# Performance work log

Measured on AMD Instinct MI355X. Metric: run time of the kernel, lower is better.

Reference implementation:

```python
import jax, jax.numpy as jnp
import numpy as np

H = 32  # d_model
EPS = 1e-5  # LayerNorm eps (PyTorch default)


def _lstm_layer(x, W_ih, W_hh, b_ih, b_hh):
    """Single LSTM layer, batch_first x: (B, T, D) -> ys: (B, T, H).
    PyTorch gate order: i, f, g, o."""
    B, T, _ = x.shape
    # Hoist the input projection out of the recurrence: one big GEMM.
    xg = jnp.einsum('btd,gd->btg', x, W_ih) + b_ih + b_hh  # (B, T, 4H)
    xg = jnp.swapaxes(xg, 0, 1)  # (T, B, 4H) for scan over time

    def step(carry, xg_t):
        h, c = carry
        gates = xg_t + h @ W_hh.T  # (B, 4H)
        i, f, g, o = jnp.split(gates, 4, axis=-1)
        i = jax.nn.sigmoid(i)
        f = jax.nn.sigmoid(f)
        g = jnp.tanh(g)
        o = jax.nn.sigmoid(o)
        c = f * c + i * g
        h = o * jnp.tanh(c)
        return (h, c), h

    h0 = jnp.zeros((B, H), dtype=x.dtype)
    c0 = jnp.zeros((B, H), dtype=x.dtype)
    (_, _), ys = jax.lax.scan(step, (h0, c0), xg)
    return jnp.swapaxes(ys, 0, 1)  # (B, T, H)


def setup_inputs() -> dict:
    key = jax.random.key(0)
    ks = jax.random.split(key, 10)
    B, T, D = 4096, 512, 6
    s = 1.0 / np.sqrt(H)  # PyTorch LSTM init scale
    inp = {
        'x': jax.random.normal(ks[0], (B, T, D), dtype=jnp.float32),
        # layer 0: input_dim=6 -> H
        'W_ih0': jax.random.uniform(ks[1], (4 * H, D), minval=-s, maxval=s, dtype=jnp.float32),
        'W_hh0': jax.random.uniform(ks[2], (4 * H, H), minval=-s, maxval=s, dtype=jnp.float32),
        'b_ih0': jax.random.uniform(ks[3], (4 * H,), minval=-s, maxval=s, dtype=jnp.float32),
        'b_hh0': jax.random.uniform(ks[4], (4 * H,), minval=-s, maxval=s, dtype=jnp.float32),
        # layer 1: H -> H
        'W_ih1': jax.random.uniform(ks[5], (4 * H, H), minval=-s, maxval=s, dtype=jnp.float32),
        'W_hh1': jax.random.uniform(ks[6], (4 * H, H), minval=-s, maxval=s, dtype=jnp.float32),
        'b_ih1': jax.random.uniform(ks[7], (4 * H,), minval=-s, maxval=s, dtype=jnp.float32),
        'b_hh1': jax.random.uniform(ks[8], (4 * H,), minval=-s, maxval=s, dtype=jnp.float32),
        # final LayerNorm params
        'ln_gamma': jnp.ones((H,), dtype=jnp.float32),
        'ln_beta': jnp.zeros((H,), dtype=jnp.float32),
    }
    return inp


def reference(x, W_ih0, W_hh0, b_ih0, b_hh0, W_ih1, W_hh1, b_ih1, b_hh1, ln_gamma, ln_beta):
    # Two-layer LSTM (dropout between layers is a no-op in eval mode).
    h1 = _lstm_layer(x, W_ih0, W_hh0, b_ih0, b_hh0)   # (B, T, H)
    h2 = _lstm_layer(h1, W_ih1, W_hh1, b_ih1, b_hh1)  # (B, T, H)
    last = h2[:, -1, :]  # (B, H)
    mu = jnp.mean(last, axis=-1, keepdims=True)
    var = jnp.var(last, axis=-1, keepdims=True)
    return (last - mu) / jnp.sqrt(var + EPS) * ln_gamma + ln_beta
```

## Files before the change

kernel.cpp:

```cpp
#include <hip/hip_runtime.h>

#define TT   512
#define DD   6
#define HD   32
#define CH   32
#define EPSL 1e-5f

typedef _Float16 half8 __attribute__((ext_vector_type(8)));
typedef __attribute__((ext_vector_type(4))) float f32x4;

#define MFMA_F16(a, b, c) __builtin_amdgcn_mfma_f32_16x16x32_f16((a), (b), (c), 0, 0, 0)

__global__ __launch_bounds__(256, 1) void lstm2_pipe(
    const float* __restrict__ x,
    const float* __restrict__ W_ih0,
    const float* __restrict__ W_hh0,
    const float* __restrict__ b_ih0,
    const float* __restrict__ b_hh0,
    const float* __restrict__ W_ih1,
    const float* __restrict__ W_hh1,
    const float* __restrict__ b_ih1,
    const float* __restrict__ b_hh1,
    const float* __restrict__ gamma,
    const float* __restrict__ beta,
    float* __restrict__ out)
{
    const int tid = threadIdx.x;
    const int w   = tid >> 6;
    const int L   = w >> 1;
    const int uh  = w & 1;
    const int ln  = tid & 63;
    const int q   = ln >> 4;
    const int n   = ln & 15;
    const int u   = 16 * uh + n;
    const int b0  = blockIdx.x << 4;

    __shared__ __align__(16) _Float16 h0r[2][16][40];
    __shared__ __align__(16) _Float16 h1r[2][16][40];
    __shared__ __align__(16) _Float16 xs[2][CH][16][8];
    __shared__ float ln_s[16][33];

    {
        unsigned* p0 = (unsigned*)&h0r[0][0][0];
        for (int i = tid; i < (int)(sizeof(h0r) / 4); i += 256) p0[i] = 0u;
        unsigned* p1 = (unsigned*)&h1r[0][0][0];
        for (int i = tid; i < (int)(sizeof(h1r) / 4); i += 256) p1[i] = 0u;
        unsigned* p2 = (unsigned*)&xs[0][0][0][0];
        for (int i = tid; i < (int)(sizeof(xs) / 4); i += 256) p2[i] = 0u;
    }

    const float* Wa = L ? W_ih1 : W_hh0;
    const float* bi = L ? b_ih1 : b_ih0;
    const float* bh = L ? b_hh1 : b_hh0;

#define SETUP(p, SC) \
    half8 Ba##p, Bb##p; float K##p; { \
        const int g = 32 * (p) + u; \
        const float4* r4 = (const float4*)(Wa + g * 32 + 8 * q); \
        float4 va = r4[0], vb = r4[1]; \
        Ba##p = half8{(_Float16)(SC * va.x), (_Float16)(SC * va.y), \
                      (_Float16)(SC * va.z), (_Float16)(SC * va.w), \
                      (_Float16)(SC * vb.x), (_Float16)(SC * vb.y), \
                      (_Float16)(SC * vb.z), (_Float16)(SC * vb.w)}; \
        Bb##p = half8{0, 0, 0, 0, 0, 0, 0, 0}; \
        if (L) { \
            const float4* s4 = (const float4*)(W_hh1 + g * 32 + 8 * q); \
            float4 sa = s4[0], sb = s4[1]; \
            Bb##p = half8{(_Float16)(SC * sa.x), (_Float16)(SC * sa.y), \
                          (_Float16)(SC * sa.z), (_Float16)(SC * sa.w), \
                          (_Float16)(SC * sb.x), (_Float16)(SC * sb.y), \
                          (_Float16)(SC * sb.z), (_Float16)(SC * sb.w)}; \
        } else if (q == 0) { \
            const float* xw = W_ih0 + g * 6; \
            Bb##p[0] = (_Float16)(SC * xw[0]); Bb##p[1] = (_Float16)(SC * xw[1]); \
            Bb##p[2] = (_Float16)(SC * xw[2]); Bb##p[3] = (_Float16)(SC * xw[3]); \
            Bb##p[4] = (_Float16)(SC * xw[4]); Bb##p[5] = (_Float16)(SC * xw[5]); \
        } \
        K##p = __builtin_amdgcn_exp2f(SC * (bi[g] + bh[g])); \
    }
    SETUP(0, -1.44269504f) SETUP(1, -1.44269504f)
    SETUP(2, -2.88539008f) SETUP(3, -1.44269504f)

    const int m0 = (tid       ) / 48, j0 = (tid       ) % 48;
    const int m1 = (tid + 256 ) / 48, j1 = (tid + 256 ) % 48;
    const int m2 = (tid + 512 ) / 48, j2 = (tid + 512 ) % 48;
    float4 xr0, xr1, xr2;

#define XLOAD(ch) { \
        const float* cb = x + (size_t)b0 * (TT * DD) + (ch) * (CH * DD); \
        xr0 = *(const float4*)(cb + (size_t)m0 * (TT * DD) + 4 * j0); \
        xr1 = *(const float4*)(cb + (size_t)m1 * (TT * DD) + 4 * j1); \
        xr2 = *(const float4*)(cb + (size_t)m2 * (TT * DD) + 4 * j2); }

#define XSTORE(buf) { \
        _Float16* xb_ = &xs[(buf)][0][0][0]; \
        { int f = 4 * j0; float4 v = xr0; \
          xb_[((f+0)/6)*128 + m0*8 + ((f+0)%6)] = (_Float16)v.x; \
          xb_[((f+1)/6)*128 + m0*8 + ((f+1)%6)] = (_Float16)v.y; \
          xb_[((f+2)/6)*128 + m0*8 + ((f+2)%6)] = (_Float16)v.z; \
          xb_[((f+3)/6)*128 + m0*8 + ((f+3)%6)] = (_Float16)v.w; } \
        { int f = 4 * j1; float4 v = xr1; \
          xb_[((f+0)/6)*128 + m1*8 + ((f+0)%6)] = (_Float16)v.x; \
          xb_[((f+1)/6)*128 + m1*8 + ((f+1)%6)] = (_Float16)v.y; \
          xb_[((f+2)/6)*128 + m1*8 + ((f+2)%6)] = (_Float16)v.z; \
          xb_[((f+3)/6)*128 + m1*8 + ((f+3)%6)] = (_Float16)v.w; } \
        { int f = 4 * j2; float4 v = xr2; \
          xb_[((f+0)/6)*128 + m2*8 + ((f+0)%6)] = (_Float16)v.x; \
          xb_[((f+1)/6)*128 + m2*8 + ((f+1)%6)] = (_Float16)v.y; \
          xb_[((f+2)/6)*128 + m2*8 + ((f+2)%6)] = (_Float16)v.z; \
          xb_[((f+3)/6)*128 + m2*8 + ((f+3)%6)] = (_Float16)v.w; } }

    XLOAD(0)
    XSTORE(0)

    float cc0 = 0.f, cc1 = 0.f, cc2 = 0.f, cc3 = 0.f;
    float hL0 = 0.f, hL1 = 0.f, hL2 = 0.f, hL3 = 0.f;

    __syncthreads();

#define GATE(p) \
    f32x4 acc##p = {0.f, 0.f, 0.f, 0.f}; \
    acc##p = MFMA_F16(Aa, Ba##p, acc##p); \
    acc##p = MFMA_F16(Ab, Bb##p, acc##p);

#define UPD(r, IS_L1, WS) { \
        float e0 = __builtin_amdgcn_exp2f(acc0[r]); \
        float e1 = __builtin_amdgcn_exp2f(acc1[r]); \
        float e2 = __builtin_amdgcn_exp2f(acc2[r]); \
        float e3 = __builtin_amdgcn_exp2f(acc3[r]); \
        float iv = __builtin_amdgcn_rcpf(fmaf(K0, e0, 1.0f)); \
        float fv = __builtin_amdgcn_rcpf(fmaf(K1, e1, 1.0f)); \
        float tg = fmaf(2.0f, __builtin_amdgcn_rcpf(fmaf(K2, e2, 1.0f)), -1.0f); \
        float ov = __builtin_amdgcn_rcpf(fmaf(K3, e3, 1.0f)); \
        cc##r = fmaf(fv, cc##r, iv * tg); \
        float ec = __builtin_amdgcn_exp2f(cc##r * -2.88539008f); \
        float tc = fmaf(2.0f, __builtin_amdgcn_rcpf(1.0f + ec), -1.0f); \
        float h_ = ov * tc; \
        if (IS_L1) { hL##r = h_; h1r[WS][4 * q + r][u] = (_Float16)h_; } \
        else       {             h0r[WS][4 * q + r][u] = (_Float16)h_; } }

#define STEP(RSL, WSL, S) \
    if (L) { \
        if ((S) >= 1 && (S) <= TT) { \
            half8 Aa = *(const half8*)&h0r[RSL][n][8 * q]; \
            half8 Ab = *(const half8*)&h1r[WSL][n][8 * q]; \
            GATE(0) GATE(1) GATE(2) GATE(3) \
            UPD(0, 1, RSL) UPD(1, 1, RSL) UPD(2, 1, RSL) UPD(3, 1, RSL) \
        } \
    } else { \
        if ((S) < TT) { \
            half8 Aa = *(const half8*)&h0r[RSL][n][8 * q]; \
            half8 Ab = half8{0, 0, 0, 0, 0, 0, 0, 0}; \
            if (q == 0) Ab = *(const half8*)&xs[((S) >> 5) & 1][(S) & (CH - 1)][n][0]; \
            GATE(0) GATE(1) GATE(2) GATE(3) \
            UPD(0, 0, WSL) UPD(1, 0, WSL) UPD(2, 0, WSL) UPD(3, 0, WSL) \
        } \
    }

    #pragma unroll 1
    for (int s = 0; s < 514; s += 2) {
        if ((s & (CH - 1)) == 0 && s < TT - CH) { XLOAD((s >> 5) + 1) }
        STEP(1, 0, s)
        __syncthreads();

        const int so = s + 1;
        STEP(0, 1, so)
        if ((so & (CH - 1)) == CH - 1 && so < TT - 1) { XSTORE(((so >> 5) + 1) & 1) }
        __syncthreads();
    }

    if (L) {
        ln_s[4 * q + 0][u] = hL0;
        ln_s[4 * q + 1][u] = hL1;
        ln_s[4 * q + 2][u] = hL2;
        ln_s[4 * q + 3][u] = hL3;
    }
    __syncthreads();

    if (tid < 16) {
        const int m = tid;
        float s = 0.f, s2 = 0.f;
        #pragma unroll
        for (int k = 0; k < HD; ++k) {
            float v = ln_s[m][k];
            s += v; s2 += v * v;
        }
        float mu  = s * (1.0f / HD);
        float var = s2 * (1.0f / HD) - mu * mu;
        float rr  = rsqrtf(var + EPSL);
        float* op = out + (size_t)(b0 + m) * HD;
        #pragma unroll
        for (int k = 0; k < HD; ++k)
            op[k] = (ln_s[m][k] - mu) * rr * gamma[k] + beta[k];
    }
}

extern "C" void kernel_launch(void* const* d_in, const int* in_sizes, int n_in,
                              void* d_out, int out_size, void* d_ws, size_t ws_size,
                              hipStream_t stream) {
    const float* x     = (const float*)d_in[0];
    const float* W_ih0 = (const float*)d_in[1];
    const float* W_hh0 = (const float*)d_in[2];
    const float* b_ih0 = (const float*)d_in[3];
    const float* b_hh0 = (const float*)d_in[4];
    const float* W_ih1 = (const float*)d_in[5];
    const float* W_hh1 = (const float*)d_in[6];
    const float* b_ih1 = (const float*)d_in[7];
    const float* b_hh1 = (const float*)d_in[8];
    const float* gamma = (const float*)d_in[9];
    const float* beta  = (const float*)d_in[10];
    float* out = (float*)d_out;

    const int B = in_sizes[0] / (TT * DD);
    lstm2_pipe<<<B / 16, 256, 0, stream>>>(x, W_ih0, W_hh0, b_ih0, b_hh0,
                                           W_ih1, W_hh1, b_ih1, b_hh1,
                                           gamma, beta, out);
}
```

Measured before the change: 330.5 us.

## Deepen layer pipeline with 4-slot h0 ring, prefetch h0, and merge reciprocals

Layer-0 hidden states now go into a 4-slot ring. Layer 1 lags by two steps and prefetches its h0 operand into a register right after computing, so the LDS read leaves the critical path between barriers. The loop is unrolled by four. The gate math is also rewritten algebraically to merge several reciprocals into fewer rcp calls, storing the cell state pre-scaled for exp2. The cost is more LDS, register pressure, and a longer pipeline drain, plus possible fp overflow risk in the combined products.

```diff
diff --git a/kernel.cpp b/kernel.cpp
--- a/kernel.cpp
+++ b/kernel.cpp
@@ -5,6 +5,8 @@
 #define HD   32
 #define CH   32
 #define EPSL 1e-5f
+#define L2E  1.44269504f
+#define L2E2 2.88539008f
 
 typedef _Float16 half8 __attribute__((ext_vector_type(8)));
 typedef __attribute__((ext_vector_type(4))) float f32x4;
@@ -35,7 +37,7 @@
     const int u   = 16 * uh + n;
     const int b0  = blockIdx.x << 4;
 
-    __shared__ __align__(16) _Float16 h0r[2][16][40];
+    __shared__ __align__(16) _Float16 h0r[4][16][40];
     __shared__ __align__(16) _Float16 h1r[2][16][40];
     __shared__ __align__(16) _Float16 xs[2][CH][16][8];
     __shared__ float ln_s[16][33];
@@ -78,8 +80,8 @@
         } \
         K##p = __builtin_amdgcn_exp2f(SC * (bi[g] + bh[g])); \
     }
-    SETUP(0, -1.44269504f) SETUP(1, -1.44269504f)
-    SETUP(2, -2.88539008f) SETUP(3, -1.44269504f)
+    SETUP(0, -L2E) SETUP(1, -L2E) SETUP(2, -L2E2) SETUP(3, -L2E)
+    const float K2c = L2E2 * K2;
 
     const int m0 = (tid       ) / 48, j0 = (tid       ) % 48;
     const int m1 = (tid + 256 ) / 48, j1 = (tid + 256 ) % 48;
@@ -115,6 +117,7 @@
 
     float cc0 = 0.f, cc1 = 0.f, cc2 = 0.f, cc3 = 0.f;
     float hL0 = 0.f, hL1 = 0.f, hL2 = 0.f, hL3 = 0.f;
+    half8 AaN = {0,0,0,0,0,0,0,0};
 
     __syncthreads();
 
@@ -128,45 +131,51 @@
         float e1 = __builtin_amdgcn_exp2f(acc1[r]); \
         float e2 = __builtin_amdgcn_exp2f(acc2[r]); \
         float e3 = __builtin_amdgcn_exp2f(acc3[r]); \
-        float iv = __builtin_amdgcn_rcpf(fmaf(K0, e0, 1.0f)); \
-        float fv = __builtin_amdgcn_rcpf(fmaf(K1, e1, 1.0f)); \
-        float tg = fmaf(2.0f, __builtin_amdgcn_rcpf(fmaf(K2, e2, 1.0f)), -1.0f); \
-        float ov = __builtin_amdgcn_rcpf(fmaf(K3, e3, 1.0f)); \
-        cc##r = fmaf(fv, cc##r, iv * tg); \
-        float ec = __builtin_amdgcn_exp2f(cc##r * -2.88539008f); \
-        float tc = fmaf(2.0f, __builtin_amdgcn_rcpf(1.0f + ec), -1.0f); \
-        float h_ = ov * tc; \
+        float pA = fmaf(K0, e0, 1.0f); \
+        float pF = fmaf(K1, e1, 1.0f); \
+        float pB = fmaf(K2, e2, 1.0f); \
+        float pO = fmaf(K3, e3, 1.0f); \
+        float Qh = fmaf(K2c, e2, -L2E2);       \
+        float P  = pA * pB; \
+        float R  = __builtin_amdgcn_rcpf(P * pF); \
+        float nm = fmaf(cc##r, P, Qh * pF); \
+        cc##r = nm * R;                         \
+        float ec = __builtin_amdgcn_exp2f(cc##r); \
+        float R2 = __builtin_amdgcn_rcpf(pO * (1.0f + ec)); \
+        float h_ = (1.0f - ec) * R2; \
         if (IS_L1) { hL##r = h_; h1r[WS][4 * q + r][u] = (_Float16)h_; } \
         else       {             h0r[WS][4 * q + r][u] = (_Float16)h_; } }
 
-#define STEP(RSL, WSL, S) \
-    if (L) { \
-        if ((S) >= 1 && (S) <= TT) { \
-            half8 Aa = *(const half8*)&h0r[RSL][n][8 * q]; \
-            half8 Ab = *(const half8*)&h1r[WSL][n][8 * q]; \
-            GATE(0) GATE(1) GATE(2) GATE(3) \
-            UPD(0, 1, RSL) UPD(1, 1, RSL) UPD(2, 1, RSL) UPD(3, 1, RSL) \
+#define BODY(J, S) { \
+        if ((J) == 0 && ((S) & (CH - 1)) == 0 && (S) < TT - CH) { XLOAD(((S) >> 5) + 1) } \
+        if (L) { \
+            if ((S) >= 2 && (S) < TT + 2) { \
+                half8 Aa = AaN; \
+                half8 Ab = *(const half8*)&h1r[((J) + 1) & 1][n][8 * q]; \
+                GATE(0) GATE(1) GATE(2) GATE(3) \
+                UPD(0, 1, (J) & 1) UPD(1, 1, (J) & 1) \
+                UPD(2, 1, (J) & 1) UPD(3, 1, (J) & 1) \
+            } \
+            AaN = *(const half8*)&h0r[((J) + 3) & 3][n][8 * q]; \
+        } else { \
+            if ((S) < TT) { \
+                half8 Aa = *(const half8*)&h0r[((J) + 3) & 3][n][8 * q]; \
+                half8 Ab = half8{0, 0, 0, 0, 0, 0, 0, 0}; \
+                if (q == 0) Ab = *(const half8*)&xs[((S) >> 5) & 1][(S) & (CH - 1)][n][0]; \
+                GATE(0) GATE(1) GATE(2) GATE(3) \
+                UPD(0, 0, (J) & 3) UPD(1, 0, (J) & 3) \
+                UPD(2, 0, (J) & 3) UPD(3, 0, (J) & 3) \
+            } \
         } \
-    } else { \
-        if ((S) < TT) { \
-            half8 Aa = *(const half8*)&h0r[RSL][n][8 * q]; \
-            half8 Ab = half8{0, 0, 0, 0, 0, 0, 0, 0}; \
-            if (q == 0) Ab = *(const half8*)&xs[((S) >> 5) & 1][(S) & (CH - 1)][n][0]; \
-            GATE(0) GATE(1) GATE(2) GATE(3) \
-            UPD(0, 0, WSL) UPD(1, 0, WSL) UPD(2, 0, WSL) UPD(3, 0, WSL) \
-        } \
-    }
+        if ((J) == 3 && (((S) & (CH - 1)) == CH - 1) && (S) < TT - 1) { XSTORE((((S) >> 5) + 1) & 1) } \
+        __syncthreads(); }
 
     #pragma unroll 1
-    for (int s = 0; s < 514; s += 2) {
-        if ((s & (CH - 1)) == 0 && s < TT - CH) { XLOAD((s >> 5) + 1) }
-        STEP(1, 0, s)
-        __syncthreads();
-
-        const int so = s + 1;
-        STEP(0, 1, so)
-        if ((so & (CH - 1)) == CH - 1 && so < TT - 1) { XSTORE(((so >> 5) + 1) & 1) }
-        __syncthreads();
+    for (int s0 = 0; s0 < 516; s0 += 4) {
+        BODY(0, s0)
+        BODY(1, s0 + 1)
+        BODY(2, s0 + 2)
+        BODY(3, s0 + 3)
     }
 
     if (L) {
```

Measured after the change: 312.3 us. 5.5% less time.
